# Optimization experiments

Hardware: AMD Instinct MI355X
Metric: run time of the kernel (lower is better)

The kernel has to match this reference:

```python
import jax, jax.numpy as jnp
import numpy as np

D_MODEL = 1024
HEADS = 16


def setup_inputs() -> dict:
    key = jax.random.key(0)
    ks = jax.random.split(key, 6)
    B, N, d = 4, 1024, D_MODEL
    s = 1.0 / np.sqrt(d)
    return {
        "x": jax.random.normal(ks[0], (B, N, d), dtype=jnp.float32),
        "attn_bias": jax.random.normal(ks[1], (B, HEADS, N, N), dtype=jnp.float32),
        "Wq": jax.random.normal(ks[2], (d, d), dtype=jnp.float32) * s,
        "Wk": jax.random.normal(ks[3], (d, d), dtype=jnp.float32) * s,
        "Wv": jax.random.normal(ks[4], (d, d), dtype=jnp.float32) * s,
        "Wo": jax.random.normal(ks[5], (d, d), dtype=jnp.float32) * s,
    }


def reference(x, attn_bias, Wq, Wk, Wv, Wo):
    B, N, d = x.shape
    H = HEADS
    hd = d // H
    # projections -> [B, H, N, hd] (torch Linear: x @ W.T)
    q = (x @ Wq.T).reshape(B, N, H, hd).transpose(0, 2, 1, 3)
    k = (x @ Wk.T).reshape(B, N, H, hd).transpose(0, 2, 1, 3)
    v = (x @ Wv.T).reshape(B, N, H, hd).transpose(0, 2, 1, 3)
    scale = hd ** -0.5
    attn = jnp.einsum('bhqd,bhkd->bhqk', q, k) * scale + attn_bias
    attn = jax.nn.softmax(attn, axis=-1)
    out = jnp.einsum('bhqk,bhkd->bhqd', attn, v)
    out = out.transpose(0, 2, 1, 3).reshape(B, N, d)
    return out @ Wo.T
```

## Files before the change

kernel.cpp:

```cpp
#include <hip/hip_runtime.h>
#include <hip/hip_bf16.h>
#include <math.h>


typedef __bf16 bf16;
typedef bf16 bf16x8 __attribute__((ext_vector_type(8)));
typedef bf16 bf16x4 __attribute__((ext_vector_type(4)));
typedef float floatx4 __attribute__((ext_vector_type(4)));

#define MFMA16(a, b, c) __builtin_amdgcn_mfma_f32_16x16x32_bf16((a), (b), (c), 0, 0, 0)

__device__ __forceinline__ void gload_lds16(const bf16* g, bf16* l) {
  __builtin_amdgcn_global_load_lds(
      (const __attribute__((address_space(1))) unsigned int*)g,
      (__attribute__((address_space(3))) unsigned int*)l, 16, 0, 0);
}

__global__ __launch_bounds__(256) void cvt_kernel(
    const float* __restrict__ x, const float* __restrict__ wq,
    const float* __restrict__ wk, const float* __restrict__ wv,
    const float* __restrict__ wo, bf16* __restrict__ dst) {
  long e = ((long)blockIdx.x * 256 + threadIdx.x) * 4;
  const float* src;
  if (e < 4194304) {
    src = x + e;
  } else {
    long r = (e - 4194304) >> 20;
    long off = (e - 4194304) & 1048575;
    src = (r == 0 ? wq : r == 1 ? wk : r == 2 ? wv : wo) + off;
  }
  float4 v = *reinterpret_cast<const float4*>(src);
  bf16x4 o = { (bf16)v.x, (bf16)v.y, (bf16)v.z, (bf16)v.w };
  *reinterpret_cast<bf16x4*>(dst + e) = o;
}

__device__ __forceinline__ void gemm_mainloop(const bf16* __restrict__ Ag,
                                              const bf16* __restrict__ Bg,
                                              bf16* As, bf16* Bs,
                                              floatx4 acc[4][4]) {
  int tid = threadIdx.x;
  int w = tid >> 6, l = tid & 63, g = l >> 4, ln = l & 15;
  int wr = (w >> 1) << 6, wc = (w & 1) << 6;
  int lrow = w * 16 + (l >> 2);
  int lkc = (l & 3) * 8;
  for (int k0 = 0; k0 < 1024; k0 += 32) {
    __syncthreads();
    gload_lds16(Ag + (size_t)lrow * 1024 + k0 + lkc, As + w * 512);
    gload_lds16(Ag + (size_t)(lrow + 64) * 1024 + k0 + lkc, As + 2048 + w * 512);
    gload_lds16(Bg + (size_t)lrow * 1024 + k0 + lkc, Bs + w * 512);
    gload_lds16(Bg + (size_t)(lrow + 64) * 1024 + k0 + lkc, Bs + 2048 + w * 512);
    asm volatile("s_waitcnt vmcnt(0)" ::: "memory");
    __syncthreads();
    bf16x8 af[4], bfv[4];
#pragma unroll
    for (int t = 0; t < 4; t++) {
      af[t] = *(const bf16x8*)&As[(wr + t * 16 + ln) * 32 + g * 8];
      bfv[t] = *(const bf16x8*)&Bs[(wc + t * 16 + ln) * 32 + g * 8];
    }
#pragma unroll
    for (int i = 0; i < 4; i++)
#pragma unroll
      for (int j = 0; j < 4; j++)
        acc[i][j] = MFMA16(af[i], bfv[j], acc[i][j]);
  }
}

__global__ __launch_bounds__(256) void qkv_proj(
    const bf16* __restrict__ xb, const bf16* __restrict__ wqkv,
    bf16* __restrict__ Qo, bf16* __restrict__ Ko, bf16* __restrict__ Vo) {
  __shared__ bf16 As[4096], Bs[4096];
  const floatx4 z4 = {0.f, 0.f, 0.f, 0.f};
  floatx4 acc[4][4];
#pragma unroll
  for (int i = 0; i < 4; i++)
#pragma unroll
    for (int j = 0; j < 4; j++) acc[i][j] = z4;
  int z = blockIdx.z;
  const bf16* Ag = xb + (size_t)blockIdx.x * 128 * 1024;
  const bf16* Bg = wqkv + (size_t)z * 1048576 + (size_t)blockIdx.y * 128 * 1024;
  gemm_mainloop(Ag, Bg, As, Bs, acc);
  bf16* dst = z == 0 ? Qo : (z == 1 ? Ko : Vo);
  int tid = threadIdx.x, w = tid >> 6, l = tid & 63, g = l >> 4, ln = l & 15;
  int mbase = blockIdx.x * 128 + ((w >> 1) << 6);
  int ibase = blockIdx.y * 128 + ((w & 1) << 6);
#pragma unroll
  for (int i = 0; i < 4; i++)
#pragma unroll
    for (int j = 0; j < 4; j++)
#pragma unroll
      for (int r = 0; r < 4; r++) {
        int m = mbase + i * 16 + g * 4 + r;
        int col = ibase + j * 16 + ln;
        int b = m >> 10, n = m & 1023, h = col >> 6, di = col & 63;
        dst[((size_t)((b * 16 + h) * 1024 + n) << 6) + di] = (bf16)acc[i][j][r];
      }
}

__global__ __launch_bounds__(256) void flash_kernel(
    const bf16* __restrict__ Q, const bf16* __restrict__ Kg,
    const bf16* __restrict__ Vg, const float* __restrict__ bias,
    bf16* __restrict__ Ao) {
  __shared__ bf16 Klds[64 * 72];
  __shared__ bf16 Vtlds[64 * 72];
  __shared__ bf16 Plds[4 * 16 * 72];
  int tid = threadIdx.x;
  int w = tid >> 6, l = tid & 63, g = l >> 4, ln = l & 15;
  int qt = blockIdx.x;
  int bh = blockIdx.y;
  size_t bhN = (size_t)bh * 1024;

  const bf16* qptr = Q + (bhN + qt * 64 + w * 16 + ln) * 64;
  bf16x8 qf0 = *(const bf16x8*)(qptr + g * 8);
  bf16x8 qf1 = *(const bf16x8*)(qptr + 32 + g * 8);

  const floatx4 z4 = {0.f, 0.f, 0.f, 0.f};
  floatx4 o[4];
  float m_i[4], l_i[4];
#pragma unroll
  for (int i = 0; i < 4; i++) { o[i] = z4; m_i[i] = -1e30f; l_i[i] = 0.f; }

  const float* bbase = bias + ((bhN + qt * 64 + w * 16 + g * 4) << 10) + ln;
  bf16* pw = Plds + w * 16 * 72;

  for (int kb = 0; kb < 16; kb++) {
    __syncthreads();
#pragma unroll
    for (int c0 = 0; c0 < 2; c0++) {
      int c = c0 * 256 + tid;
      int key = c >> 3, kc = c & 7;
      const bf16* kp = Kg + (bhN + kb * 64 + key) * 64 + kc * 8;
      *(bf16x8*)&Klds[key * 72 + kc * 8] = *(const bf16x8*)kp;
      bf16x8 vv = *(const bf16x8*)(Vg + (bhN + kb * 64 + key) * 64 + kc * 8);
#pragma unroll
      for (int j = 0; j < 8; j++) Vtlds[(kc * 8 + j) * 72 + key] = vv[j];
    }
    __syncthreads();

    floatx4 s[4];
#pragma unroll
    for (int t = 0; t < 4; t++) {
      s[t] = z4;
      bf16x8 kf0 = *(const bf16x8*)&Klds[(t * 16 + ln) * 72 + g * 8];
      bf16x8 kf1 = *(const bf16x8*)&Klds[(t * 16 + ln) * 72 + 32 + g * 8];
      s[t] = MFMA16(qf0, kf0, s[t]);
      s[t] = MFMA16(qf1, kf1, s[t]);
    }
    const float* bp = bbase + kb * 64;
#pragma unroll
    for (int t = 0; t < 4; t++)
#pragma unroll
      for (int r = 0; r < 4; r++)
        s[t][r] = fmaf(s[t][r], 0.125f, bp[(size_t)r * 1024 + t * 16]);

    float cmax[4], rs[4], alpha[4];
#pragma unroll
    for (int r = 0; r < 4; r++)
      cmax[r] = fmaxf(fmaxf(s[0][r], s[1][r]), fmaxf(s[2][r], s[3][r]));
#pragma unroll
    for (int mk = 1; mk < 16; mk <<= 1)
#pragma unroll
      for (int r = 0; r < 4; r++)
        cmax[r] = fmaxf(cmax[r], __shfl_xor(cmax[r], mk, 64));
#pragma unroll
    for (int r = 0; r < 4; r++) {
      float mn = fmaxf(m_i[r], cmax[r]);
      alpha[r] = __expf(m_i[r] - mn);
      m_i[r] = mn;
      rs[r] = 0.f;
    }
#pragma unroll
    for (int t = 0; t < 4; t++)
#pragma unroll
      for (int r = 0; r < 4; r++) {
        float p = __expf(s[t][r] - m_i[r]);
        s[t][r] = p;
        rs[r] += p;
      }
#pragma unroll
    for (int mk = 1; mk < 16; mk <<= 1)
#pragma unroll
      for (int r = 0; r < 4; r++) rs[r] += __shfl_xor(rs[r], mk, 64);
#pragma unroll
    for (int r = 0; r < 4; r++) l_i[r] = l_i[r] * alpha[r] + rs[r];
#pragma unroll
    for (int dt = 0; dt < 4; dt++)
#pragma unroll
      for (int r = 0; r < 4; r++) o[dt][r] *= alpha[r];

#pragma unroll
    for (int t = 0; t < 4; t++)
#pragma unroll
      for (int r = 0; r < 4; r++)
        pw[(g * 4 + r) * 72 + t * 16 + ln] = (bf16)s[t][r];
    asm volatile("s_waitcnt lgkmcnt(0)" ::: "memory");

    bf16x8 pf0 = *(const bf16x8*)&pw[ln * 72 + g * 8];
    bf16x8 pf1 = *(const bf16x8*)&pw[ln * 72 + 32 + g * 8];
#pragma unroll
    for (int dt = 0; dt < 4; dt++) {
      bf16x8 vf0 = *(const bf16x8*)&Vtlds[(dt * 16 + ln) * 72 + g * 8];
      bf16x8 vf1 = *(const bf16x8*)&Vtlds[(dt * 16 + ln) * 72 + 32 + g * 8];
      o[dt] = MFMA16(pf0, vf0, o[dt]);
      o[dt] = MFMA16(pf1, vf1, o[dt]);
    }
  }

  int b = bh >> 4, h = bh & 15;
#pragma unroll
  for (int r = 0; r < 4; r++) {
    float inv = 1.f / l_i[r];
    int row = b * 1024 + qt * 64 + w * 16 + g * 4 + r;
    bf16* op = Ao + (size_t)row * 1024 + h * 64 + ln;
#pragma unroll
    for (int dt = 0; dt < 4; dt++) op[dt * 16] = (bf16)(o[dt][r] * inv);
  }
}

__global__ __launch_bounds__(256) void out_proj(const bf16* __restrict__ Ab,
                                                const bf16* __restrict__ wob,
                                                float* __restrict__ C) {
  __shared__ bf16 As[4096], Bs[4096];
  const floatx4 z4 = {0.f, 0.f, 0.f, 0.f};
  floatx4 acc[4][4];
#pragma unroll
  for (int i = 0; i < 4; i++)
#pragma unroll
    for (int j = 0; j < 4; j++) acc[i][j] = z4;
  const bf16* Ag = Ab + (size_t)blockIdx.x * 128 * 1024;
  const bf16* Bg = wob + (size_t)blockIdx.y * 128 * 1024;
  gemm_mainloop(Ag, Bg, As, Bs, acc);
  int tid = threadIdx.x, w = tid >> 6, l = tid & 63, g = l >> 4, ln = l & 15;
  int mbase = blockIdx.x * 128 + ((w >> 1) << 6);
  int cbase = blockIdx.y * 128 + ((w & 1) << 6);
#pragma unroll
  for (int i = 0; i < 4; i++)
#pragma unroll
    for (int j = 0; j < 4; j++)
#pragma unroll
      for (int r = 0; r < 4; r++)
        C[(size_t)(mbase + i * 16 + g * 4 + r) * 1024 + cbase + j * 16 + ln] =
            acc[i][j][r];
}

extern "C" void kernel_launch(void* const* d_in, const int* in_sizes, int n_in,
                              void* d_out, int out_size, void* d_ws, size_t ws_size,
                              hipStream_t stream) {
  const float* x = (const float*)d_in[0];
  const float* bias = (const float*)d_in[1];
  const float* Wq = (const float*)d_in[2];
  const float* Wk = (const float*)d_in[3];
  const float* Wv = (const float*)d_in[4];
  const float* Wo = (const float*)d_in[5];
  float* out = (float*)d_out;

  bf16* xb = (bf16*)d_ws;
  bf16* wqkv = xb + 4194304;
  bf16* wob = wqkv + 3 * 1048576;
  bf16* Qb = wob + 1048576;
  bf16* Kb = Qb + 4194304;
  bf16* Vb = Kb + 4194304;
  bf16* Ao = Vb + 4194304;

  cvt_kernel<<<8192, 256, 0, stream>>>(x, Wq, Wk, Wv, Wo, xb);
  qkv_proj<<<dim3(32, 8, 3), 256, 0, stream>>>(xb, wqkv, Qb, Kb, Vb);
  flash_kernel<<<dim3(16, 64), 256, 0, stream>>>(Qb, Kb, Vb, bias, Ao);
  out_proj<<<dim3(32, 8), 256, 0, stream>>>(Ao, wob, out);
}
```

Before: 477.8 us.

## Prefetch attention bias a tile ahead and shrink out-proj tile to 128x64

In the flash kernel, the fp32 attention-bias values for the next key block are loaded into registers before the QK MFMAs of the current block. This hides global-load latency on the largest input stream. The K/V staging index mapping is also changed so each thread handles one key row and two chunks. The output projection now uses 128x64 tiles with its own inline mainloop, doubling the grid to 512 blocks for better CU occupancy, at the cost of more A-tile reloads and extra register pressure from the bias buffers.

```diff
diff --git a/kernel.cpp b/kernel.cpp
--- a/kernel.cpp
+++ b/kernel.cpp
@@ -120,21 +120,38 @@
   for (int i = 0; i < 4; i++) { o[i] = z4; m_i[i] = -1e30f; l_i[i] = 0.f; }
 
   const float* bbase = bias + ((bhN + qt * 64 + w * 16 + g * 4) << 10) + ln;
+  float bc[4][4];
+#pragma unroll
+  for (int t = 0; t < 4; t++)
+#pragma unroll
+    for (int r = 0; r < 4; r++) bc[t][r] = bbase[(size_t)r * 1024 + t * 16];
+
   bf16* pw = Plds + w * 16 * 72;
+  int skey = l;
+  int skc2 = w * 2;
 
   for (int kb = 0; kb < 16; kb++) {
     __syncthreads();
+    const bf16* krow = Kg + (bhN + kb * 64 + skey) * 64;
+    const bf16* vrow = Vg + (bhN + kb * 64 + skey) * 64;
 #pragma unroll
     for (int c0 = 0; c0 < 2; c0++) {
-      int c = c0 * 256 + tid;
-      int key = c >> 3, kc = c & 7;
-      const bf16* kp = Kg + (bhN + kb * 64 + key) * 64 + kc * 8;
-      *(bf16x8*)&Klds[key * 72 + kc * 8] = *(const bf16x8*)kp;
-      bf16x8 vv = *(const bf16x8*)(Vg + (bhN + kb * 64 + key) * 64 + kc * 8);
-#pragma unroll
-      for (int j = 0; j < 8; j++) Vtlds[(kc * 8 + j) * 72 + key] = vv[j];
-    }
-    __syncthreads();
+      int kc = skc2 + c0;
+      *(bf16x8*)&Klds[skey * 72 + kc * 8] = *(const bf16x8*)(krow + kc * 8);
+      bf16x8 vv = *(const bf16x8*)(vrow + kc * 8);
+#pragma unroll
+      for (int j = 0; j < 8; j++) Vtlds[(kc * 8 + j) * 72 + skey] = vv[j];
+    }
+    __syncthreads();
+
+    float bn[4][4];
+    if (kb < 15) {
+      const float* bp = bbase + (kb + 1) * 64;
+#pragma unroll
+      for (int t = 0; t < 4; t++)
+#pragma unroll
+        for (int r = 0; r < 4; r++) bn[t][r] = bp[(size_t)r * 1024 + t * 16];
+    }
 
     floatx4 s[4];
 #pragma unroll
@@ -145,12 +162,11 @@
       s[t] = MFMA16(qf0, kf0, s[t]);
       s[t] = MFMA16(qf1, kf1, s[t]);
     }
-    const float* bp = bbase + kb * 64;
 #pragma unroll
     for (int t = 0; t < 4; t++)
 #pragma unroll
       for (int r = 0; r < 4; r++)
-        s[t][r] = fmaf(s[t][r], 0.125f, bp[(size_t)r * 1024 + t * 16]);
+        s[t][r] = fmaf(s[t][r], 0.125f, bc[t][r]);
 
     float cmax[4], rs[4], alpha[4];
 #pragma unroll
@@ -203,6 +219,10 @@
       o[dt] = MFMA16(pf0, vf0, o[dt]);
       o[dt] = MFMA16(pf1, vf1, o[dt]);
     }
+#pragma unroll
+    for (int t = 0; t < 4; t++)
+#pragma unroll
+      for (int r = 0; r < 4; r++) bc[t][r] = bn[t][r];
   }
 
   int b = bh >> 4, h = bh & 15;
@@ -219,23 +239,46 @@
 __global__ __launch_bounds__(256) void out_proj(const bf16* __restrict__ Ab,
                                                 const bf16* __restrict__ wob,
                                                 float* __restrict__ C) {
-  __shared__ bf16 As[4096], Bs[4096];
+  __shared__ bf16 As[4096], Bs[2048];
   const floatx4 z4 = {0.f, 0.f, 0.f, 0.f};
-  floatx4 acc[4][4];
+  floatx4 acc[4][2];
 #pragma unroll
   for (int i = 0; i < 4; i++)
 #pragma unroll
-    for (int j = 0; j < 4; j++) acc[i][j] = z4;
+    for (int j = 0; j < 2; j++) acc[i][j] = z4;
   const bf16* Ag = Ab + (size_t)blockIdx.x * 128 * 1024;
-  const bf16* Bg = wob + (size_t)blockIdx.y * 128 * 1024;
-  gemm_mainloop(Ag, Bg, As, Bs, acc);
-  int tid = threadIdx.x, w = tid >> 6, l = tid & 63, g = l >> 4, ln = l & 15;
-  int mbase = blockIdx.x * 128 + ((w >> 1) << 6);
-  int cbase = blockIdx.y * 128 + ((w & 1) << 6);
+  const bf16* Bg = wob + (size_t)blockIdx.y * 64 * 1024;
+  int tid = threadIdx.x;
+  int w = tid >> 6, l = tid & 63, g = l >> 4, ln = l & 15;
+  int wr = (w >> 1) << 6, wc = (w & 1) << 5;
+  int lrow = w * 16 + (l >> 2);
+  int lkc = (l & 3) * 8;
+  for (int k0 = 0; k0 < 1024; k0 += 32) {
+    __syncthreads();
+    gload_lds16(Ag + (size_t)lrow * 1024 + k0 + lkc, As + w * 512);
+    gload_lds16(Ag + (size_t)(lrow + 64) * 1024 + k0 + lkc, As + 2048 + w * 512);
+    gload_lds16(Bg + (size_t)lrow * 1024 + k0 + lkc, Bs + w * 512);
+    asm volatile("s_waitcnt vmcnt(0)" ::: "memory");
+    __syncthreads();
+    bf16x8 af[4], bfv[2];
+#pragma unroll
+    for (int t = 0; t < 4; t++)
+      af[t] = *(const bf16x8*)&As[(wr + t * 16 + ln) * 32 + g * 8];
+#pragma unroll
+    for (int t = 0; t < 2; t++)
+      bfv[t] = *(const bf16x8*)&Bs[(wc + t * 16 + ln) * 32 + g * 8];
+#pragma unroll
+    for (int i = 0; i < 4; i++)
+#pragma unroll
+      for (int j = 0; j < 2; j++)
+        acc[i][j] = MFMA16(af[i], bfv[j], acc[i][j]);
+  }
+  int mbase = blockIdx.x * 128 + wr;
+  int cbase = blockIdx.y * 64 + wc;
 #pragma unroll
   for (int i = 0; i < 4; i++)
 #pragma unroll
-    for (int j = 0; j < 4; j++)
+    for (int j = 0; j < 2; j++)
 #pragma unroll
       for (int r = 0; r < 4; r++)
         C[(size_t)(mbase + i * 16 + g * 4 + r) * 1024 + cbase + j * 16 + ln] =
@@ -264,5 +307,5 @@
   cvt_kernel<<<8192, 256, 0, stream>>>(x, Wq, Wk, Wv, Wo, xb);
   qkv_proj<<<dim3(32, 8, 3), 256, 0, stream>>>(xb, wqkv, Qb, Kb, Vb);
   flash_kernel<<<dim3(16, 64), 256, 0, stream>>>(Qb, Kb, Vb, bias, Ao);
-  out_proj<<<dim3(32, 8), 256, 0, stream>>>(Ao, wob, out);
-}
+  out_proj<<<dim3(32, 16), 256, 0, stream>>>(Ao, wob, out);
+}
```

Result: slower. 504.0 us (+5.5%).
